# Kernel optimization log

Measured on AMD Instinct MI355X. Metric: run time of the kernel, lower is better.

Reference implementation:

```python
import jax, jax.numpy as jnp
import numpy as np

B, N, D, H, L = 1024, 500, 128, 8, 2  # batch, nb_nodes, dim_emb, nb_heads, nb_layers_decoder
CLIP = 10.0


def _mha(q, K, V, h, mask, clip):
    # q: (B,1,D) single query; K,V: (B,N,D); mask: (B,N) True = forbidden
    Bsz, Nn, Dd = K.shape
    dh = Dd // h
    qh = q.reshape(Bsz, h, dh)            # head k takes contiguous chunk of dim_emb (matches torch view)
    Kh = K.reshape(Bsz, Nn, h, dh)
    Vh = V.reshape(Bsz, Nn, h, dh)
    scores = jnp.einsum('bhd,bnhd->bhn', qh, Kh) / jnp.sqrt(jnp.asarray(dh, q.dtype))
    if clip is not None:
        scores = clip * jnp.tanh(scores)
    scores = jnp.where(mask[:, None, :], jnp.asarray(-1e9, scores.dtype), scores)
    w = jax.nn.softmax(scores, axis=-1)   # (B,h,N)
    out = jnp.einsum('bhn,bnhd->bhd', w, Vh).reshape(Bsz, 1, Dd)
    return out, w.mean(axis=1, keepdims=True)  # (B,1,D), (B,1,N)


def setup_inputs() -> dict:
    key = jax.random.key(0)
    ks = jax.random.split(key, 8)
    query = jax.random.normal(ks[0], (B, 1, D), dtype=jnp.float32)
    K_att = jax.random.normal(ks[1], (B, N, D * L), dtype=jnp.float32)
    V_att = jax.random.normal(ks[2], (B, N, D * L), dtype=jnp.float32)
    mask = jax.random.bernoulli(ks[3], 0.3, (B, N))
    mask = mask.at[:, 0].set(False)  # guarantee every row has a legal action
    s = 1.0 / np.sqrt(D)
    W0_w = jax.random.normal(ks[4], (D, D), dtype=jnp.float32) * s
    W0_b = jnp.zeros((D,), dtype=jnp.float32)
    Wq_w = jax.random.normal(ks[5], (D, D), dtype=jnp.float32) * s
    Wq_b = jnp.zeros((D,), dtype=jnp.float32)
    return {"query": query, "K_att": K_att, "V_att": V_att, "mask": mask,
            "W0_w": W0_w, "W0_b": W0_b, "Wq_w": Wq_w, "Wq_b": Wq_b}


def reference(query, K_att, V_att, mask, W0_w, W0_b, Wq_w, Wq_b):
    q = query
    attn_w = None
    for l in range(L):
        Kl = K_att[:, :, l * D:(l + 1) * D]
        Vl = V_att[:, :, l * D:(l + 1) * D]
        if l < L - 1:
            out, _ = _mha(q, Kl, Vl, H, mask, None)
            q = out @ W0_w.T + W0_b
        else:
            qf = q @ Wq_w.T + Wq_b
            _, attn_w = _mha(qf, Kl, Vl, 1, mask, CLIP)
    return attn_w[:, 0, :]  # (B, N) prob of next node
```

## Files before the change

### kernel.cpp

```cpp
#include <hip/hip_runtime.h>
#include <hip/hip_bf16.h>
#include <math.h>

constexpr int NKEY = 500;
constexpr int DIM = 128;
constexpr int HEADS = 8;
constexpr int ROWSTRIDE = 256;

__global__ __launch_bounds__(256)
void fused_pomo_attn(const float* __restrict__ query,
                     const float* __restrict__ K_att,
                     const float* __restrict__ V_att,
                     const int*   __restrict__ mask,
                     const float* __restrict__ W0_w,
                     const float* __restrict__ W0_b,
                     const float* __restrict__ Wq_w,
                     const float* __restrict__ Wq_b,
                     float* __restrict__ out)
{
    const int b = blockIdx.x;
    const int tid = threadIdx.x;
    const int lane32 = tid & 31;
    const int grp = tid >> 5;

    __shared__ alignas(16) float s_sc[HEADS][NKEY];
    __shared__ alignas(16) float s_red[8][DIM];
    __shared__ alignas(16) float s_out[DIM];
    __shared__ alignas(16) float s_q1[DIM];
    __shared__ alignas(16) float s_qf[DIM];
    __shared__ alignas(16) float s_s1[NKEY];
    __shared__ int s_idx[NKEY];
    __shared__ int s_cnt;
    __shared__ float s_m[4], s_l[4];

    const size_t brow = (size_t)b * NKEY;

    if (tid < 64) {
        int off = 0;
        for (int base = 0; base < NKEY; base += 64) {
            const int n = base + tid;
            const bool keep = (n < NKEY) && (mask[brow + n] == 0);
            const unsigned long long bal = __ballot(keep);
            const int pre = __popcll(bal & ((1ull << tid) - 1ull));
            if (keep) s_idx[off + pre] = n;
            off += __popcll(bal);
        }
        if (tid == 0) s_cnt = off;
    }
    __syncthreads();
    const int M = s_cnt;

    const float4 q4 = ((const float4*)(query + (size_t)b * DIM))[lane32];
    for (int base = 0; base < M; base += 16) {
        const int p0 = base + grp;
        const int p1 = base + 8 + grp;
        const bool ok0 = p0 < M, ok1 = p1 < M;
        const int n0 = ok0 ? s_idx[p0] : 0;
        const int n1 = ok1 ? s_idx[p1] : 0;
        float4 k0 = make_float4(0.f,0.f,0.f,0.f), k1 = make_float4(0.f,0.f,0.f,0.f);
        if (ok0) k0 = ((const float4*)(K_att + (brow + n0) * ROWSTRIDE))[lane32];
        if (ok1) k1 = ((const float4*)(K_att + (brow + n1) * ROWSTRIDE))[lane32];
        float s0 = q4.x*k0.x + q4.y*k0.y + q4.z*k0.z + q4.w*k0.w;
        float s1 = q4.x*k1.x + q4.y*k1.y + q4.z*k1.z + q4.w*k1.w;
        s0 += __shfl_xor(s0, 1); s0 += __shfl_xor(s0, 2);
        s1 += __shfl_xor(s1, 1); s1 += __shfl_xor(s1, 2);
        if ((lane32 & 3) == 0) {
            const int h = lane32 >> 2;
            if (ok0) s_sc[h][p0] = s0 * 0.25f;
            if (ok1) s_sc[h][p1] = s1 * 0.25f;
        }
    }
    __syncthreads();

    {
        float m = -INFINITY;
        for (int p = lane32; p < M; p += 32) m = fmaxf(m, s_sc[grp][p]);
        #pragma unroll
        for (int o = 16; o > 0; o >>= 1) m = fmaxf(m, __shfl_xor(m, o));
        float l = 0.f;
        for (int p = lane32; p < M; p += 32) {
            const float e = __expf(s_sc[grp][p] - m);
            s_sc[grp][p] = e;
            l += e;
        }
        #pragma unroll
        for (int o = 16; o > 0; o >>= 1) l += __shfl_xor(l, o);
        const float inv = 1.f / l;
        for (int p = lane32; p < M; p += 32) s_sc[grp][p] *= inv;
    }
    __syncthreads();

    {
        float4 acc = make_float4(0.f, 0.f, 0.f, 0.f);
        const int h = lane32 >> 2;
        for (int base = 0; base < M; base += 16) {
            const int p0 = base + grp;
            const int p1 = base + 8 + grp;
            const bool ok0 = p0 < M, ok1 = p1 < M;
            const int n0 = ok0 ? s_idx[p0] : 0;
            const int n1 = ok1 ? s_idx[p1] : 0;
            float4 v0 = make_float4(0.f,0.f,0.f,0.f), v1 = make_float4(0.f,0.f,0.f,0.f);
            if (ok0) v0 = ((const float4*)(V_att + (brow + n0) * ROWSTRIDE))[lane32];
            if (ok1) v1 = ((const float4*)(V_att + (brow + n1) * ROWSTRIDE))[lane32];
            const float w0 = ok0 ? s_sc[h][p0] : 0.f;
            const float w1 = ok1 ? s_sc[h][p1] : 0.f;
            acc.x += w0 * v0.x + w1 * v1.x;
            acc.y += w0 * v0.y + w1 * v1.y;
            acc.z += w0 * v0.z + w1 * v1.z;
            acc.w += w0 * v0.w + w1 * v1.w;
        }
        ((float4*)s_red[grp])[lane32] = acc;
    }
    __syncthreads();
    if (tid < DIM) {
        float v = 0.f;
        #pragma unroll
        for (int g = 0; g < 8; g++) v += s_red[g][tid];
        s_out[tid] = v;
    }
    __syncthreads();

    {
        const int i = tid >> 1, half = tid & 1;
        const float4* wrow = (const float4*)(W0_w + (size_t)i * DIM + half * 64);
        float ssum = 0.f;
        #pragma unroll
        for (int k = 0; k < 16; k++) {
            const float4 w4 = wrow[k];
            const float4 o4 = ((const float4*)s_out)[half * 16 + k];
            ssum += w4.x*o4.x + w4.y*o4.y + w4.z*o4.z + w4.w*o4.w;
        }
        ssum += __shfl_xor(ssum, 1);
        if (half == 0) s_q1[i] = ssum + W0_b[i];
    }
    __syncthreads();

    {
        const int i = tid >> 1, half = tid & 1;
        const float4* wrow = (const float4*)(Wq_w + (size_t)i * DIM + half * 64);
        float ssum = 0.f;
        #pragma unroll
        for (int k = 0; k < 16; k++) {
            const float4 w4 = wrow[k];
            const float4 o4 = ((const float4*)s_q1)[half * 16 + k];
            ssum += w4.x*o4.x + w4.y*o4.y + w4.z*o4.z + w4.w*o4.w;
        }
        ssum += __shfl_xor(ssum, 1);
        if (half == 0) s_qf[i] = ssum + Wq_b[i];
    }
    __syncthreads();

    {
        const float4 qf4 = ((const float4*)s_qf)[lane32];
        for (int base = 0; base < M; base += 16) {
            const int p0 = base + grp;
            const int p1 = base + 8 + grp;
            const bool ok0 = p0 < M, ok1 = p1 < M;
            const int n0 = ok0 ? s_idx[p0] : 0;
            const int n1 = ok1 ? s_idx[p1] : 0;
            float4 k0 = make_float4(0.f,0.f,0.f,0.f), k1 = make_float4(0.f,0.f,0.f,0.f);
            if (ok0) k0 = ((const float4*)(K_att + (brow + n0) * ROWSTRIDE + DIM))[lane32];
            if (ok1) k1 = ((const float4*)(K_att + (brow + n1) * ROWSTRIDE + DIM))[lane32];
            float s0 = qf4.x*k0.x + qf4.y*k0.y + qf4.z*k0.z + qf4.w*k0.w;
            float s1 = qf4.x*k1.x + qf4.y*k1.y + qf4.z*k1.z + qf4.w*k1.w;
            #pragma unroll
            for (int o = 1; o < 32; o <<= 1) { s0 += __shfl_xor(s0, o); s1 += __shfl_xor(s1, o); }
            if (lane32 == 0) {
                if (ok0) s_s1[p0] = 10.f * tanhf(s0 * 0.08838834764831845f);
                if (ok1) s_s1[p1] = 10.f * tanhf(s1 * 0.08838834764831845f);
            }
        }
    }
    for (int n = tid; n < NKEY; n += 256) out[brow + n] = 0.f;
    __syncthreads();

    {
        const int wid = tid >> 6;
        const int lane = tid & 63;
        float m = -INFINITY;
        for (int p = tid; p < M; p += 256) m = fmaxf(m, s_s1[p]);
        #pragma unroll
        for (int o = 32; o > 0; o >>= 1) m = fmaxf(m, __shfl_xor(m, o));
        if (lane == 0) s_m[wid] = m;
        __syncthreads();
        m = fmaxf(fmaxf(s_m[0], s_m[1]), fmaxf(s_m[2], s_m[3]));
        float l = 0.f;
        for (int p = tid; p < M; p += 256) {
            const float e = __expf(s_s1[p] - m);
            s_s1[p] = e;
            l += e;
        }
        #pragma unroll
        for (int o = 32; o > 0; o >>= 1) l += __shfl_xor(l, o);
        if (lane == 0) s_l[wid] = l;
        __syncthreads();
        l = s_l[0] + s_l[1] + s_l[2] + s_l[3];
        const float inv = 1.f / l;
        for (int p = tid; p < M; p += 256) out[brow + s_idx[p]] = s_s1[p] * inv;
    }
}

extern "C" void kernel_launch(void* const* d_in, const int* in_sizes, int n_in,
                              void* d_out, int out_size, void* d_ws, size_t ws_size,
                              hipStream_t stream) {
    const float* query = (const float*)d_in[0];
    const float* K_att = (const float*)d_in[1];
    const float* V_att = (const float*)d_in[2];
    const int*   mask  = (const int*)d_in[3];
    const float* W0_w  = (const float*)d_in[4];
    const float* W0_b  = (const float*)d_in[5];
    const float* Wq_w  = (const float*)d_in[6];
    const float* Wq_b  = (const float*)d_in[7];
    float* out = (float*)d_out;

    const int B = in_sizes[0] / DIM;
    fused_pomo_attn<<<B, 256, 0, stream>>>(query, K_att, V_att, mask,
                                           W0_w, W0_b, Wq_w, Wq_b, out);
}
```

Before: 122.7 us.

## Fuse layer-0 score and value passes with online softmax; unroll final scoring

```diff
diff --git a/kernel.cpp b/kernel.cpp
--- a/kernel.cpp
+++ b/kernel.cpp
@@ -4,7 +4,6 @@
 
 constexpr int NKEY = 500;
 constexpr int DIM = 128;
-constexpr int HEADS = 8;
 constexpr int ROWSTRIDE = 256;
 
 __global__ __launch_bounds__(256)
@@ -23,8 +22,9 @@
     const int lane32 = tid & 31;
     const int grp = tid >> 5;
 
-    __shared__ alignas(16) float s_sc[HEADS][NKEY];
     __shared__ alignas(16) float s_red[8][DIM];
+    __shared__ float s_m8[8][32];
+    __shared__ float s_l8[8][32];
     __shared__ alignas(16) float s_out[DIM];
     __shared__ alignas(16) float s_q1[DIM];
     __shared__ alignas(16) float s_qf[DIM];
@@ -50,73 +50,55 @@
     __syncthreads();
     const int M = s_cnt;
 
-    const float4 q4 = ((const float4*)(query + (size_t)b * DIM))[lane32];
-    for (int base = 0; base < M; base += 16) {
-        const int p0 = base + grp;
-        const int p1 = base + 8 + grp;
-        const bool ok0 = p0 < M, ok1 = p1 < M;
-        const int n0 = ok0 ? s_idx[p0] : 0;
-        const int n1 = ok1 ? s_idx[p1] : 0;
-        float4 k0 = make_float4(0.f,0.f,0.f,0.f), k1 = make_float4(0.f,0.f,0.f,0.f);
-        if (ok0) k0 = ((const float4*)(K_att + (brow + n0) * ROWSTRIDE))[lane32];
-        if (ok1) k1 = ((const float4*)(K_att + (brow + n1) * ROWSTRIDE))[lane32];
-        float s0 = q4.x*k0.x + q4.y*k0.y + q4.z*k0.z + q4.w*k0.w;
-        float s1 = q4.x*k1.x + q4.y*k1.y + q4.z*k1.z + q4.w*k1.w;
-        s0 += __shfl_xor(s0, 1); s0 += __shfl_xor(s0, 2);
-        s1 += __shfl_xor(s1, 1); s1 += __shfl_xor(s1, 2);
-        if ((lane32 & 3) == 0) {
-            const int h = lane32 >> 2;
-            if (ok0) s_sc[h][p0] = s0 * 0.25f;
-            if (ok1) s_sc[h][p1] = s1 * 0.25f;
-        }
-    }
-    __syncthreads();
-
-    {
-        float m = -INFINITY;
-        for (int p = lane32; p < M; p += 32) m = fmaxf(m, s_sc[grp][p]);
-        #pragma unroll
-        for (int o = 16; o > 0; o >>= 1) m = fmaxf(m, __shfl_xor(m, o));
-        float l = 0.f;
-        for (int p = lane32; p < M; p += 32) {
-            const float e = __expf(s_sc[grp][p] - m);
-            s_sc[grp][p] = e;
-            l += e;
-        }
-        #pragma unroll
-        for (int o = 16; o > 0; o >>= 1) l += __shfl_xor(l, o);
-        const float inv = 1.f / l;
-        for (int p = lane32; p < M; p += 32) s_sc[grp][p] *= inv;
-    }
-    __syncthreads();
-
-    {
+    {
+        const float4 q4 = ((const float4*)(query + (size_t)b * DIM))[lane32];
+        float m = -1e30f, l = 0.f;
         float4 acc = make_float4(0.f, 0.f, 0.f, 0.f);
-        const int h = lane32 >> 2;
         for (int base = 0; base < M; base += 16) {
             const int p0 = base + grp;
             const int p1 = base + 8 + grp;
             const bool ok0 = p0 < M, ok1 = p1 < M;
             const int n0 = ok0 ? s_idx[p0] : 0;
             const int n1 = ok1 ? s_idx[p1] : 0;
-            float4 v0 = make_float4(0.f,0.f,0.f,0.f), v1 = make_float4(0.f,0.f,0.f,0.f);
-            if (ok0) v0 = ((const float4*)(V_att + (brow + n0) * ROWSTRIDE))[lane32];
-            if (ok1) v1 = ((const float4*)(V_att + (brow + n1) * ROWSTRIDE))[lane32];
-            const float w0 = ok0 ? s_sc[h][p0] : 0.f;
-            const float w1 = ok1 ? s_sc[h][p1] : 0.f;
-            acc.x += w0 * v0.x + w1 * v1.x;
-            acc.y += w0 * v0.y + w1 * v1.y;
-            acc.z += w0 * v0.z + w1 * v1.z;
-            acc.w += w0 * v0.w + w1 * v1.w;
+            const float4 k0 = ((const float4*)(K_att + (brow + n0) * ROWSTRIDE))[lane32];
+            const float4 k1 = ((const float4*)(K_att + (brow + n1) * ROWSTRIDE))[lane32];
+            const float4 v0 = ((const float4*)(V_att + (brow + n0) * ROWSTRIDE))[lane32];
+            const float4 v1 = ((const float4*)(V_att + (brow + n1) * ROWSTRIDE))[lane32];
+            float s0 = q4.x*k0.x + q4.y*k0.y + q4.z*k0.z + q4.w*k0.w;
+            float s1 = q4.x*k1.x + q4.y*k1.y + q4.z*k1.z + q4.w*k1.w;
+            s0 += __shfl_xor(s0, 1); s0 += __shfl_xor(s0, 2);
+            s1 += __shfl_xor(s1, 1); s1 += __shfl_xor(s1, 2);
+            s0 = ok0 ? s0 * 0.25f : -1e30f;
+            s1 = ok1 ? s1 * 0.25f : -1e30f;
+            const float m2 = fmaxf(m, fmaxf(s0, s1));
+            const float f  = __expf(m - m2);
+            const float w0 = ok0 ? __expf(s0 - m2) : 0.f;
+            const float w1 = ok1 ? __expf(s1 - m2) : 0.f;
+            l = l * f + w0 + w1;
+            acc.x = acc.x * f + w0 * v0.x + w1 * v1.x;
+            acc.y = acc.y * f + w0 * v0.y + w1 * v1.y;
+            acc.z = acc.z * f + w0 * v0.z + w1 * v1.z;
+            acc.w = acc.w * f + w0 * v0.w + w1 * v1.w;
+            m = m2;
         }
         ((float4*)s_red[grp])[lane32] = acc;
+        s_m8[grp][lane32] = m;
+        s_l8[grp][lane32] = l;
     }
     __syncthreads();
     if (tid < DIM) {
-        float v = 0.f;
-        #pragma unroll
-        for (int g = 0; g < 8; g++) v += s_red[g][tid];
-        s_out[tid] = v;
+        const int ql = tid >> 2;
+        float M_ = -1e30f;
+        #pragma unroll
+        for (int g = 0; g < 8; g++) M_ = fmaxf(M_, s_m8[g][ql]);
+        float L = 0.f, o = 0.f;
+        #pragma unroll
+        for (int g = 0; g < 8; g++) {
+            const float f = __expf(s_m8[g][ql] - M_);
+            L += s_l8[g][ql] * f;
+            o += s_red[g][tid] * f;
+        }
+        s_out[tid] = o / L;
     }
     __syncthreads();
 
@@ -152,22 +134,34 @@
 
     {
         const float4 qf4 = ((const float4*)s_qf)[lane32];
-        for (int base = 0; base < M; base += 16) {
+        for (int base = 0; base < M; base += 32) {
             const int p0 = base + grp;
-            const int p1 = base + 8 + grp;
-            const bool ok0 = p0 < M, ok1 = p1 < M;
+            const int p1 = base + 8  + grp;
+            const int p2 = base + 16 + grp;
+            const int p3 = base + 24 + grp;
+            const bool ok0 = p0 < M, ok1 = p1 < M, ok2 = p2 < M, ok3 = p3 < M;
             const int n0 = ok0 ? s_idx[p0] : 0;
             const int n1 = ok1 ? s_idx[p1] : 0;
-            float4 k0 = make_float4(0.f,0.f,0.f,0.f), k1 = make_float4(0.f,0.f,0.f,0.f);
-            if (ok0) k0 = ((const float4*)(K_att + (brow + n0) * ROWSTRIDE + DIM))[lane32];
-            if (ok1) k1 = ((const float4*)(K_att + (brow + n1) * ROWSTRIDE + DIM))[lane32];
+            const int n2 = ok2 ? s_idx[p2] : 0;
+            const int n3 = ok3 ? s_idx[p3] : 0;
+            const float4 k0 = ((const float4*)(K_att + (brow + n0) * ROWSTRIDE + DIM))[lane32];
+            const float4 k1 = ((const float4*)(K_att + (brow + n1) * ROWSTRIDE + DIM))[lane32];
+            const float4 k2 = ((const float4*)(K_att + (brow + n2) * ROWSTRIDE + DIM))[lane32];
+            const float4 k3 = ((const float4*)(K_att + (brow + n3) * ROWSTRIDE + DIM))[lane32];
             float s0 = qf4.x*k0.x + qf4.y*k0.y + qf4.z*k0.z + qf4.w*k0.w;
             float s1 = qf4.x*k1.x + qf4.y*k1.y + qf4.z*k1.z + qf4.w*k1.w;
+            float s2 = qf4.x*k2.x + qf4.y*k2.y + qf4.z*k2.z + qf4.w*k2.w;
+            float s3 = qf4.x*k3.x + qf4.y*k3.y + qf4.z*k3.z + qf4.w*k3.w;
             #pragma unroll
-            for (int o = 1; o < 32; o <<= 1) { s0 += __shfl_xor(s0, o); s1 += __shfl_xor(s1, o); }
+            for (int o = 1; o < 32; o <<= 1) {
+                s0 += __shfl_xor(s0, o); s1 += __shfl_xor(s1, o);
+                s2 += __shfl_xor(s2, o); s3 += __shfl_xor(s3, o);
+            }
             if (lane32 == 0) {
                 if (ok0) s_s1[p0] = 10.f * tanhf(s0 * 0.08838834764831845f);
                 if (ok1) s_s1[p1] = 10.f * tanhf(s1 * 0.08838834764831845f);
+                if (ok2) s_s1[p2] = 10.f * tanhf(s2 * 0.08838834764831845f);
+                if (ok3) s_s1[p3] = 10.f * tanhf(s3 * 0.08838834764831845f);
             }
         }
     }
```

Result: no change. 121.2 us (-1.2%).
